# Kernel tuning notes

Hardware: AMD Instinct MI355X
Metric: run time of the kernel (lower is better)

## Reference

```python
import jax, jax.numpy as jnp
import numpy as np

B, N, D, C, NCLS = 8, 2048, 256, 128, 50
EPS = 1e-5  # BatchNorm eps

def _bn(x, g, b):
    # eval-mode BatchNorm1d over channel dim of (B,C,N): running_mean=0, running_var=1
    return x * (g / jnp.sqrt(1.0 + EPS))[:, None] + b[:, None]

def _complex_linear(x, Wr, br, Wi, bi):
    # torch ComplexLinear: complex(fr(x.real)-fi(x.imag), fr(x.imag)+fi(x.real))
    xr, xi = x.real, x.imag
    re = (xr @ Wr.T + br) - (xi @ Wi.T + bi)
    im = (xi @ Wr.T + br) + (xr @ Wi.T + bi)
    return jax.lax.complex(re, im)

def _sa(x, qkW, vW, vb, tW, tb, g, b):
    # x: (B,C,N); q/k share weights (tied in torch), dim C//4
    xq = jnp.einsum('qc,bcn->bnq', qkW, x)            # (B,N,C/4)
    xk = jnp.einsum('qc,bcm->bqm', qkW, x)            # (B,C/4,N)
    energy = jnp.einsum('bnq,bqm->bnm', xq, xk)       # (B,N,N)
    attn = jax.nn.softmax(energy, axis=-1)
    attn = attn / (1e-9 + attn.sum(axis=1, keepdims=True))  # column renorm
    xv = jnp.einsum('oc,bcn->bon', vW, x) + vb[:, None]
    xr = x - jnp.einsum('bcn,bnm->bcm', xv, attn)
    xr = jnp.einsum('oc,bcn->bon', tW, xr) + tb[:, None]
    return x + jax.nn.relu(_bn(xr, g, b))

def reference(xyz, cls_label, A, Bmat, W1r, b1r, W1i, b1i, W2r, b2r, W2i, b2i,
              lbl_emb, ft_w1, ft_g1, ft_b1, ft_w2, ft_g2, ft_b2,
              sa_qk, sa_vw, sa_vb, sa_tw, sa_tb, sa_g, sa_b,
              fuse_w, fuse_g, fuse_b, c1_w, c1_b, bn1_g, bn1_b, c2_w, c2_b):
    pts = xyz.transpose(0, 2, 1)                       # (B,N,3)
    # VecKM(d=256, alpha=30, beta=9): G = eB (eB^H eA), normalized to sqrt(d)
    eA = jnp.exp(1j * (pts @ A))                       # (B,N,D) complex64
    eB = jnp.exp(1j * (pts @ Bmat))
    inner = jnp.einsum('bnd,bne->bde', eB.conj(), eA)  # (B,D,D)
    G = jnp.einsum('bnd,bde->bne', eB, inner)          # (B,N,D)
    G = G / jnp.linalg.norm(G, axis=-1, keepdims=True) * jnp.sqrt(jnp.float32(D))
    G = _complex_linear(G, W1r, b1r, W1i, b1i)
    G = jax.lax.complex(jax.nn.relu(G.real), jax.nn.relu(G.imag))  # ComplexReLU
    G = _complex_linear(G, W2r, b2r, W2i, b2i)
    G = (G.real ** 2 + G.imag ** 2).transpose(0, 2, 1)  # (B,D,N)
    reweight = (cls_label @ lbl_emb)[:, :, None]        # (B,D,1)
    x = G * reweight
    x = jax.nn.relu(_bn(jnp.einsum('oc,bcn->bon', ft_w1, x), ft_g1, ft_b1))
    x = _bn(jnp.einsum('oc,bcn->bon', ft_w2, x), ft_g2, ft_b2)  # (B,C,N)
    feats = []
    for i in range(4):
        x = _sa(x, sa_qk[i], sa_vw[i], sa_vb[i], sa_tw[i], sa_tb[i], sa_g[i], sa_b[i])
        feats.append(x)
    x = jnp.concatenate(feats, axis=1)                  # (B,4C,N)
    x = jax.nn.relu(_bn(jnp.einsum('oc,bcn->bon', fuse_w, x), fuse_g, fuse_b))
    x = jax.nn.relu(_bn(jnp.einsum('oc,bcn->bon', c1_w, x) + c1_b[:, None], bn1_g, bn1_b))
    # dropout is identity in eval mode
    x = jnp.einsum('oc,bcn->bon', c2_w, x) + c2_b[:, None]
    x = jax.nn.log_softmax(x, axis=1)
    return x.transpose(0, 2, 1)                         # (B,N,NCLS)

def setup_inputs():
    key = jax.random.key(0)
    k = jax.random.split(key, 24)
    rn = lambda i, s: jax.random.normal(k[i], s, jnp.float32)
    s = 0.05
    return {
        'xyz': rn(0, (B, 3, N)),
        'cls_label': jax.random.uniform(k[1], (B, 16), jnp.float32),
        'A': rn(2, (3, D)) * 30.0,
        'Bmat': rn(3, (3, D)) * 9.0,
        'W1r': rn(4, (D, D)) * s, 'b1r': rn(5, (D,)) * s,
        'W1i': rn(6, (D, D)) * s, 'b1i': rn(7, (D,)) * s,
        'W2r': rn(8, (D, D)) * s, 'b2r': rn(9, (D,)) * s,
        'W2i': rn(10, (D, D)) * s, 'b2i': rn(11, (D,)) * s,
        'lbl_emb': rn(12, (16, D)),
        'ft_w1': rn(13, (C, D)) * s, 'ft_g1': jnp.ones((C,)), 'ft_b1': jnp.zeros((C,)),
        'ft_w2': rn(14, (C, C)) * s, 'ft_g2': jnp.ones((C,)), 'ft_b2': jnp.zeros((C,)),
        'sa_qk': rn(15, (4, C // 4, C)) * s,
        'sa_vw': rn(16, (4, C, C)) * s, 'sa_vb': rn(17, (4, C)) * s,
        'sa_tw': rn(18, (4, C, C)) * s, 'sa_tb': rn(19, (4, C)) * s,
        'sa_g': jnp.ones((4, C)), 'sa_b': jnp.zeros((4, C)),
        'fuse_w': rn(20, (C, 4 * C)) * s, 'fuse_g': jnp.ones((C,)), 'fuse_b': jnp.zeros((C,)),
        'c1_w': rn(21, (C, C)) * s, 'c1_b': rn(22, (C,)) * s,
        'bn1_g': jnp.ones((C,)), 'bn1_b': jnp.zeros((C,)),
        'c2_w': rn(23, (NCLS, C)) * s, 'c2_b': jnp.zeros((NCLS,)),
    }
```

## Files before the change

kernel.cpp:

```cpp
#include <hip/hip_runtime.h>

#define BB 8
#define NPTS 2048
#define DD 256
#define CCH 128
#define NCLASS 50
#define LOG2E 1.4426950408889634f

typedef __attribute__((ext_vector_type(8))) short short8;
typedef __attribute__((ext_vector_type(4))) float f32x4;
typedef unsigned short u16;
#define MFMA16(a,b,c) __builtin_amdgcn_mfma_f32_16x16x32_bf16(a,b,c,0,0,0)

__device__ __forceinline__ u16 f2bf(float x){
  union { float f; unsigned int u; } v; v.f = x;
  unsigned int r = v.u + 0x7FFFu + ((v.u >> 16) & 1u);
  return (u16)(r >> 16);
}
__device__ __forceinline__ float bf2f(u16 u){
  union { unsigned int u32; float f; } v; v.u32 = ((unsigned int)u) << 16; return v.f;
}
__device__ __forceinline__ void split2(float x, u16& h, u16& l){
  h = f2bf(x); l = f2bf(x - bf2f(h));
}
__device__ __forceinline__ short8 ld8(const u16* p){ return *(const short8*)p; }
__device__ __forceinline__ short8 zero8(){ short8 z = {0,0,0,0,0,0,0,0}; return z; }
__device__ __forceinline__ void split8(const float* v, short8& H, short8& L){
  #pragma unroll
  for (int i = 0; i < 8; i++) { u16 h, l; split2(v[i], h, l); H[i] = (short)h; L[i] = (short)l; }
}

struct WSplit {
  const float* src[12];
  int cnt[12];
  int off[12];
};
__global__ __launch_bounds__(256) void wsplit_kernel(WSplit wsp, u16* __restrict__ H,
                                                     u16* __restrict__ L)
{
  int seg = blockIdx.y;
  int idx = blockIdx.x*256 + threadIdx.x;
  if (idx >= wsp.cnt[seg]) return;
  float v = wsp.src[seg][idx];
  u16 h, l; split2(v, h, l);
  H[wsp.off[seg]+idx] = h; L[wsp.off[seg]+idx] = l;
}

__global__ __launch_bounds__(256) void ek1_kernel(
    const float* __restrict__ xyz, const float* __restrict__ A, const float* __restrict__ Bm,
    u16* __restrict__ ATrh, u16* __restrict__ ATrl, u16* __restrict__ ATih, u16* __restrict__ ATil,
    u16* __restrict__ BTrh, u16* __restrict__ BTrl, u16* __restrict__ BTih, u16* __restrict__ BTil)
{
  size_t idx = (size_t)blockIdx.x*256 + threadIdx.x;
  int n = (int)(idx & (NPTS-1));
  int d = (int)((idx >> 11) & (DD-1));
  int b = (int)(idx >> 19);
  float p0 = xyz[((size_t)b*3+0)*NPTS+n];
  float p1 = xyz[((size_t)b*3+1)*NPTS+n];
  float p2 = xyz[((size_t)b*3+2)*NPTS+n];
  float phA = p0*A[d] + p1*A[DD+d] + p2*A[2*DD+d];
  float phB = p0*Bm[d] + p1*Bm[DD+d] + p2*Bm[2*DD+d];
  float sa, ca, sb, cb;
  sincosf(phA, &sa, &ca);
  sincosf(phB, &sb, &cb);
  size_t off = ((size_t)b*DD + d)*NPTS + n;
  u16 h, l;
  split2(ca, h, l); ATrh[off] = h; ATrl[off] = l;
  split2(sa, h, l); ATih[off] = h; ATil[off] = l;
  split2(cb, h, l); BTrh[off] = h; BTrl[off] = l;
  split2(sb, h, l); BTih[off] = h; BTil[off] = l;
}

__global__ __launch_bounds__(256) void ek2_kernel(
    const float* __restrict__ xyz, const float* __restrict__ Bm,
    u16* __restrict__ Brh, u16* __restrict__ Brl, u16* __restrict__ Bih, u16* __restrict__ Bil)
{
  size_t idx = (size_t)blockIdx.x*256 + threadIdx.x;
  int d = (int)(idx & (DD-1));
  int n = (int)((idx >> 8) & (NPTS-1));
  int b = (int)(idx >> 19);
  float p0 = xyz[((size_t)b*3+0)*NPTS+n];
  float p1 = xyz[((size_t)b*3+1)*NPTS+n];
  float p2 = xyz[((size_t)b*3+2)*NPTS+n];
  float phB = p0*Bm[d] + p1*Bm[DD+d] + p2*Bm[2*DD+d];
  float sb, cb;
  sincosf(phB, &sb, &cb);
  size_t off = ((size_t)b*NPTS + n)*DD + d;
  u16 h, l;
  split2(cb, h, l); Brh[off] = h; Brl[off] = l;
  split2(sb, h, l); Bih[off] = h; Bil[off] = l;
}

__global__ __launch_bounds__(256) void inner_mfma_kernel(
    const u16* __restrict__ ATrh, const u16* __restrict__ ATrl,
    const u16* __restrict__ ATih, const u16* __restrict__ ATil,
    const u16* __restrict__ BTrh, const u16* __restrict__ BTrl,
    const u16* __restrict__ BTih, const u16* __restrict__ BTil,
    float2* __restrict__ PART)
{
  int z = blockIdx.z; int b = z & 7; int ch = z >> 3;
  int e0 = blockIdx.y*64, d0 = blockIdx.x*64;
  int tid = threadIdx.x, lane = tid & 63, w = tid >> 6;
  int wr = (w >> 1)*32, wc = (w & 1)*32;
  int r16 = lane & 15, g4 = lane >> 4;
  f32x4 re[2][2] = {}, ip[2][2] = {}, iq[2][2] = {};
  size_t ar_[2], br_[2];
  #pragma unroll
  for (int rg = 0; rg < 2; rg++) {
    ar_[rg] = ((size_t)b*DD + (e0 + wr + rg*16 + r16))*NPTS + g4*8;
    br_[rg] = ((size_t)b*DD + (d0 + wc + rg*16 + r16))*NPTS + g4*8;
  }
  int kbeg = ch*512, kend = kbeg + 512;
  for (int k0 = kbeg; k0 < kend; k0 += 32) {
    short8 arh[2], arl[2], aih[2], ail[2], brh[2], brl[2], bih[2], bil[2];
    #pragma unroll
    for (int rg = 0; rg < 2; rg++) {
      arh[rg] = ld8(ATrh + ar_[rg] + k0); arl[rg] = ld8(ATrl + ar_[rg] + k0);
      aih[rg] = ld8(ATih + ar_[rg] + k0); ail[rg] = ld8(ATil + ar_[rg] + k0);
      brh[rg] = ld8(BTrh + br_[rg] + k0); brl[rg] = ld8(BTrl + br_[rg] + k0);
      bih[rg] = ld8(BTih + br_[rg] + k0); bil[rg] = ld8(BTil + br_[rg] + k0);
    }
    #pragma unroll
    for (int ra = 0; ra < 2; ra++)
      #pragma unroll
      for (int rb = 0; rb < 2; rb++) {
        re[ra][rb] = MFMA16(arh[ra], brh[rb], re[ra][rb]);
        re[ra][rb] = MFMA16(arh[ra], brl[rb], re[ra][rb]);
        re[ra][rb] = MFMA16(arl[ra], brh[rb], re[ra][rb]);
        re[ra][rb] = MFMA16(aih[ra], bih[rb], re[ra][rb]);
        re[ra][rb] = MFMA16(aih[ra], bil[rb], re[ra][rb]);
        re[ra][rb] = MFMA16(ail[ra], bih[rb], re[ra][rb]);
        ip[ra][rb] = MFMA16(aih[ra], brh[rb], ip[ra][rb]);
        ip[ra][rb] = MFMA16(aih[ra], brl[rb], ip[ra][rb]);
        ip[ra][rb] = MFMA16(ail[ra], brh[rb], ip[ra][rb]);
        iq[ra][rb] = MFMA16(arh[ra], bih[rb], iq[ra][rb]);
        iq[ra][rb] = MFMA16(arh[ra], bil[rb], iq[ra][rb]);
        iq[ra][rb] = MFMA16(arl[ra], bih[rb], iq[ra][rb]);
      }
  }
  float2* outp = PART + ((size_t)(ch*BB + b)*DD)*DD;
  #pragma unroll
  for (int ra = 0; ra < 2; ra++)
    #pragma unroll
    for (int rb = 0; rb < 2; rb++)
      #pragma unroll
      for (int j = 0; j < 4; j++) {
        int e = e0 + wr + ra*16 + g4*4 + j;
        int d = d0 + wc + rb*16 + r16;
        outp[(size_t)e*DD + d] = make_float2(re[ra][rb][j], ip[ra][rb][j] - iq[ra][rb][j]);
      }
}

__global__ __launch_bounds__(256) void innred_kernel(const float2* __restrict__ P,
    u16* __restrict__ Irh, u16* __restrict__ Irl, u16* __restrict__ Iih, u16* __restrict__ Iil)
{
  size_t i = (size_t)blockIdx.x*256 + threadIdx.x;
  const size_t S = (size_t)BB*DD*DD;
  float2 a = P[i], b = P[i+S], c = P[i+2*S], d = P[i+3*S];
  float rr = a.x+b.x+c.x+d.x, ii = a.y+b.y+c.y+d.y;
  u16 h, l;
  split2(rr, h, l); Irh[i] = h; Irl[i] = l;
  split2(ii, h, l); Iih[i] = h; Iil[i] = l;
}

__global__ __launch_bounds__(256) void g_mfma_kernel(
    const u16* __restrict__ Brh, const u16* __restrict__ Brl,
    const u16* __restrict__ Bih, const u16* __restrict__ Bil,
    const u16* __restrict__ Irh, const u16* __restrict__ Irl,
    const u16* __restrict__ Iih, const u16* __restrict__ Iil,
    float2* __restrict__ G)
{
  int b = blockIdx.z;
  int n0 = blockIdx.y*64, e0 = blockIdx.x*64;
  int tid = threadIdx.x, lane = tid & 63, w = tid >> 6;
  int wr = (w >> 1)*32, wc = (w & 1)*32;
  int r16 = lane & 15, g4 = lane >> 4;
  f32x4 p[2][2] = {}, q[2][2] = {}, im[2][2] = {};
  size_t ar_[2], br_[2];
  #pragma unroll
  for (int rg = 0; rg < 2; rg++) {
    ar_[rg] = ((size_t)b*NPTS + (n0 + wr + rg*16 + r16))*DD + g4*8;
    br_[rg] = ((size_t)b*DD + (e0 + wc + rg*16 + r16))*DD + g4*8;
  }
  for (int k0 = 0; k0 < DD; k0 += 32) {
    short8 arh[2], arl[2], aih[2], ail[2], brh[2], brl[2], bih[2], bil[2];
    #pragma unroll
    for (int rg = 0; rg < 2; rg++) {
      arh[rg] = ld8(Brh + ar_[rg] + k0); arl[rg] = ld8(Brl + ar_[rg] + k0);
      aih[rg] = ld8(Bih + ar_[rg] + k0); ail[rg] = ld8(Bil + ar_[rg] + k0);
      brh[rg] = ld8(Irh + br_[rg] + k0); brl[rg] = ld8(Irl + br_[rg] + k0);
      bih[rg] = ld8(Iih + br_[rg] + k0); bil[rg] = ld8(Iil + br_[rg] + k0);
    }
    #pragma unroll
    for (int ra = 0; ra < 2; ra++)
      #pragma unroll
      for (int rb = 0; rb < 2; rb++) {
        p[ra][rb] = MFMA16(arh[ra], brh[rb], p[ra][rb]);
        p[ra][rb] = MFMA16(arh[ra], brl[rb], p[ra][rb]);
        p[ra][rb] = MFMA16(arl[ra], brh[rb], p[ra][rb]);
        q[ra][rb] = MFMA16(aih[ra], bih[rb], q[ra][rb]);
        q[ra][rb] = MFMA16(aih[ra], bil[rb], q[ra][rb]);
        q[ra][rb] = MFMA16(ail[ra], bih[rb], q[ra][rb]);
        im[ra][rb] = MFMA16(arh[ra], bih[rb], im[ra][rb]);
        im[ra][rb] = MFMA16(arh[ra], bil[rb], im[ra][rb]);
        im[ra][rb] = MFMA16(arl[ra], bih[rb], im[ra][rb]);
        im[ra][rb] = MFMA16(aih[ra], brh[rb], im[ra][rb]);
        im[ra][rb] = MFMA16(aih[ra], brl[rb], im[ra][rb]);
        im[ra][rb] = MFMA16(ail[ra], brh[rb], im[ra][rb]);
      }
  }
  #pragma unroll
  for (int ra = 0; ra < 2; ra++)
    #pragma unroll
    for (int rb = 0; rb < 2; rb++)
      #pragma unroll
      for (int j = 0; j < 4; j++) {
        int n = n0 + wr + ra*16 + g4*4 + j;
        int e = e0 + wc + rb*16 + r16;
        G[((size_t)b*NPTS + n)*DD + e] = make_float2(p[ra][rb][j] - q[ra][rb][j], im[ra][rb][j]);
      }
}

__global__ __launch_bounds__(256) void gnorm_kernel(float2* __restrict__ G)
{
  size_t row = blockIdx.x;
  float2* p = G + row*DD;
  int tid = threadIdx.x;
  float2 v = p[tid];
  __shared__ float red[256];
  red[tid] = v.x*v.x + v.y*v.y;
  __syncthreads();
  for (int w = 128; w > 0; w >>= 1) { if (tid < w) red[tid] += red[tid+w]; __syncthreads(); }
  float sc = 16.f * rsqrtf(red[0]);
  p[tid] = make_float2(v.x*sc, v.y*sc);
}

__global__ __launch_bounds__(256) void clinear_mfma_kernel(
    const float2* __restrict__ IN,
    const u16* __restrict__ Wrh, const u16* __restrict__ Wrl,
    const u16* __restrict__ Wih, const u16* __restrict__ Wil,
    const float* __restrict__ br, const float* __restrict__ bi,
    float2* __restrict__ OUT, int do_relu)
{
  int m0 = blockIdx.y*64, o0 = blockIdx.x*64;
  int tid = threadIdx.x, lane = tid & 63, w = tid >> 6;
  int wr = (w >> 1)*32, wc = (w & 1)*32;
  int r16 = lane & 15, g4 = lane >> 4;
  f32x4 p[2][2] = {}, q[2][2] = {}, im[2][2] = {};
  int mrow[2], orow[2];
  #pragma unroll
  for (int rg = 0; rg < 2; rg++) {
    mrow[rg] = m0 + wr + rg*16 + r16;
    orow[rg] = o0 + wc + rg*16 + r16;
  }
  for (int k0 = 0; k0 < DD; k0 += 32) {
    short8 arh[2], arl[2], aih[2], ail[2], brh[2], brl[2], bih[2], bil[2];
    #pragma unroll
    for (int rg = 0; rg < 2; rg++) {
      const float2* pa = IN + (size_t)mrow[rg]*DD + k0 + g4*8;
      float vr[8], vi[8];
      #pragma unroll
      for (int j = 0; j < 8; j++) { float2 t = pa[j]; vr[j] = t.x; vi[j] = t.y; }
      split8(vr, arh[rg], arl[rg]); split8(vi, aih[rg], ail[rg]);
      size_t wo = (size_t)orow[rg]*DD + k0 + g4*8;
      brh[rg] = ld8(Wrh + wo); brl[rg] = ld8(Wrl + wo);
      bih[rg] = ld8(Wih + wo); bil[rg] = ld8(Wil + wo);
    }
    #pragma unroll
    for (int ra = 0; ra < 2; ra++)
      #pragma unroll
      for (int rb = 0; rb < 2; rb++) {
        p[ra][rb] = MFMA16(arh[ra], brh[rb], p[ra][rb]);
        p[ra][rb] = MFMA16(arh[ra], brl[rb], p[ra][rb]);
        p[ra][rb] = MFMA16(arl[ra], brh[rb], p[ra][rb]);
        q[ra][rb] = MFMA16(aih[ra], bih[rb], q[ra][rb]);
        q[ra][rb] = MFMA16(aih[ra], bil[rb], q[ra][rb]);
        q[ra][rb] = MFMA16(ail[ra], bih[rb], q[ra][rb]);
        im[ra][rb] = MFMA16(arh[ra], bih[rb], im[ra][rb]);
        im[ra][rb] = MFMA16(arh[ra], bil[rb], im[ra][rb]);
        im[ra][rb] = MFMA16(arl[ra], bih[rb], im[ra][rb]);
        im[ra][rb] = MFMA16(aih[ra], brh[rb], im[ra][rb]);
        im[ra][rb] = MFMA16(aih[ra], brl[rb], im[ra][rb]);
        im[ra][rb] = MFMA16(ail[ra], brh[rb], im[ra][rb]);
      }
  }
  #pragma unroll
  for (int ra = 0; ra < 2; ra++)
    #pragma unroll
    for (int rb = 0; rb < 2; rb++)
      #pragma unroll
      for (int j = 0; j < 4; j++) {
        int m = m0 + wr + ra*16 + g4*4 + j;
        int o = o0 + wc + rb*16 + r16;
        float brv = br[o], biv = bi[o];
        float re = p[ra][rb][j] - q[ra][rb][j] + brv - biv;
        float iv = im[ra][rb][j] + brv + biv;
        if (do_relu) { re = fmaxf(re, 0.f); iv = fmaxf(iv, 0.f); }
        OUT[(size_t)m*DD + o] = make_float2(re, iv);
      }
}

__global__ void rw_kernel(const float* __restrict__ cls, const float* __restrict__ lbl,
                          float* __restrict__ RW)
{
  int b = blockIdx.x; int d = threadIdx.x;
  float s = 0.f;
  #pragma unroll
  for (int k = 0; k < 16; k++) s += cls[b*16+k] * lbl[k*DD+d];
  RW[b*DD+d] = s;
}

__global__ __launch_bounds__(256) void gsq_kernel(
    const float2* __restrict__ G, const float* __restrict__ RW, float* __restrict__ OUT)
{
  size_t idx = (size_t)blockIdx.x*256 + threadIdx.x;
  int d = (int)(idx & (DD-1));
  size_t bn = idx >> 8;
  int n = (int)(bn & (NPTS-1));
  int b = (int)(bn >> 11);
  float2 g = G[idx];
  OUT[((size_t)b*DD + d)*NPTS + n] = (g.x*g.x + g.y*g.y) * RW[b*DD+d];
}

__global__ __launch_bounds__(256) void sgemm_kernel(
    const u16* __restrict__ Wh, const u16* __restrict__ Wl,
    const float* __restrict__ X, float* __restrict__ Y,
    const float* __restrict__ RES,
    const float* __restrict__ bias, const float* __restrict__ bng, const float* __restrict__ bnb,
    u16* __restrict__ YBh, u16* __restrict__ YBl, int ybmode,
    int O, int Cin, size_t xbs, size_t ybs, size_t rbs, int flags)
{
  int b = blockIdx.z;
  int n0 = blockIdx.x*64, o0 = blockIdx.y*64;
  const float* x = X + (size_t)b*xbs;
  __shared__ u16 sXh[64][40], sXl[64][40];
  int tid = threadIdx.x, lane = tid & 63, w = tid >> 6;
  int wo = (w >> 1)*32, wn = (w & 1)*32;
  int r16 = lane & 15, g4 = lane >> 4;
  f32x4 acc[2][2] = {};
  int stc = tid >> 3;
  int stn = (tid & 7)*8;
  for (int k0 = 0; k0 < Cin; k0 += 32) {
    const float* px = x + (size_t)(k0+stc)*NPTS + n0 + stn;
    float4 u0 = *(const float4*)px;
    float4 u1 = *(const float4*)(px+4);
    float v[8] = {u0.x,u0.y,u0.z,u0.w,u1.x,u1.y,u1.z,u1.w};
    __syncthreads();
    #pragma unroll
    for (int j = 0; j < 8; j++) {
      u16 h, l; split2(v[j], h, l);
      sXh[stn+j][stc] = h; sXl[stn+j][stc] = l;
    }
    __syncthreads();
    short8 awh[2], awl[2], bxh[2], bxl[2];
    #pragma unroll
    for (int rg = 0; rg < 2; rg++) {
      int orow = o0 + wo + rg*16 + r16;
      if (orow < O) {
        size_t woff = (size_t)orow*Cin + k0 + g4*8;
        awh[rg] = ld8(Wh + woff); awl[rg] = ld8(Wl + woff);
      } else { awh[rg] = zero8(); awl[rg] = zero8(); }
      bxh[rg] = ld8(&sXh[wn + rg*16 + r16][g4*8]);
      bxl[rg] = ld8(&sXl[wn + rg*16 + r16][g4*8]);
    }
    #pragma unroll
    for (int ra = 0; ra < 2; ra++)
      #pragma unroll
      for (int rb = 0; rb < 2; rb++) {
        acc[ra][rb] = MFMA16(awh[ra], bxh[rb], acc[ra][rb]);
        acc[ra][rb] = MFMA16(awh[ra], bxl[rb], acc[ra][rb]);
        acc[ra][rb] = MFMA16(awl[ra], bxh[rb], acc[ra][rb]);
      }
  }
  #pragma unroll
  for (int ra = 0; ra < 2; ra++)
    #pragma unroll
    for (int rb = 0; rb < 2; rb++)
      #pragma unroll
      for (int j = 0; j < 4; j++) {
        int o = o0 + wo + ra*16 + g4*4 + j;
        if (o >= O) continue;
        int n = n0 + wn + rb*16 + r16;
        float v = acc[ra][rb][j];
        if (flags & 1) v += bias[o];
        if (flags & 2) v = v * (bng[o] * rsqrtf(1.f + 1e-5f)) + bnb[o];
        if (flags & 4) v = fmaxf(v, 0.f);
        if (flags & 8) v += RES[(size_t)b*rbs + (size_t)o*NPTS + n];
        if (ybmode == 0) Y[(size_t)b*ybs + (size_t)o*NPTS + n] = v;
        else if (ybmode == 1) YBh[(size_t)b*ybs + (size_t)o*NPTS + n] = f2bf(v);
        else {
          u16 h, l; split2(v, h, l);
          size_t off = ((size_t)b*NPTS + n)*32 + o;
          YBh[off] = h; YBl[off] = l;
        }
      }
}

__global__ __launch_bounds__(256) void sastat_kernel(
    const u16* __restrict__ Qh, const u16* __restrict__ Ql,
    float* __restrict__ PM, float* __restrict__ PS)
{
  int b = blockIdx.z, ch = blockIdx.y;
  int n0 = blockIdx.x*64;
  size_t base = (size_t)b*NPTS*32;
  int tid = threadIdx.x, lane = tid & 63, wid = tid >> 6;
  int r16 = lane & 15, g4 = lane >> 4;
  size_t ao = base + (size_t)(n0 + wid*16 + r16)*32 + g4*8;
  short8 ah = ld8(Qh + ao), al = ld8(Ql + ao);
  float pm[4] = {-3.4e38f,-3.4e38f,-3.4e38f,-3.4e38f};
  float ps[4] = {0.f,0.f,0.f,0.f};
  int mbeg = ch*512, mend = mbeg + 512;
  for (int mt = mbeg; mt < mend; mt += 32) {
    size_t bo0 = base + (size_t)(mt + r16)*32 + g4*8;
    size_t bo1 = bo0 + 16*32;
    short8 bh0 = ld8(Qh+bo0), bl0 = ld8(Ql+bo0);
    short8 bh1 = ld8(Qh+bo1), bl1 = ld8(Ql+bo1);
    f32x4 a0 = {}, a1 = {};
    a0 = MFMA16(ah, bh0, a0); a0 = MFMA16(ah, bl0, a0); a0 = MFMA16(al, bh0, a0);
    a1 = MFMA16(ah, bh1, a1); a1 = MFMA16(ah, bl1, a1); a1 = MFMA16(al, bh1, a1);
    #pragma unroll
    for (int j = 0; j < 4; j++) {
      float v = fmaxf(a0[j], a1[j]);
      float mn = fmaxf(pm[j], v);
      ps[j] = ps[j]*exp2f((pm[j]-mn)*LOG2E)
            + exp2f((a0[j]-mn)*LOG2E) + exp2f((a1[j]-mn)*LOG2E);
      pm[j] = mn;
    }
  }
  #pragma unroll
  for (int j = 0; j < 4; j++) {
    float m = pm[j], s = ps[j];
    #pragma unroll
    for (int d = 1; d < 16; d <<= 1) {
      float om = __shfl_xor(m, d);
      float os = __shfl_xor(s, d);
      float mn = fmaxf(m, om);
      s = s*exp2f((m-mn)*LOG2E) + os*exp2f((om-mn)*LOG2E);
      m = mn;
    }
    if (r16 == 0) {
      int n_ = n0 + wid*16 + g4*4 + j;
      size_t off = ((size_t)ch*BB + b)*NPTS + n_;
      PM[off] = m; PS[off] = s;
    }
  }
}

__global__ __launch_bounds__(256) void comb1_kernel(
    const float* __restrict__ PM, const float* __restrict__ PS,
    float* __restrict__ MX, float* __restrict__ RS)
{
  size_t i = (size_t)blockIdx.x*256 + threadIdx.x;
  const size_t S = (size_t)BB*NPTS;
  float m0 = PM[i], m1 = PM[i+S], m2 = PM[i+2*S], m3 = PM[i+3*S];
  float mx = fmaxf(fmaxf(m0,m1), fmaxf(m2,m3));
  float den = PS[i]*exp2f((m0-mx)*LOG2E) + PS[i+S]*exp2f((m1-mx)*LOG2E)
            + PS[i+2*S]*exp2f((m2-mx)*LOG2E) + PS[i+3*S]*exp2f((m3-mx)*LOG2E);
  MX[i] = mx; RS[i] = 1.f/den;
}

__global__ __launch_bounds__(256) void saattn_kernel(
    const u16* __restrict__ Qh, const u16* __restrict__ Ql,
    const float* __restrict__ MX, const float* __restrict__ RS,
    u16* __restrict__ AT, float* __restrict__ CSP)
{
  int b = blockIdx.z, ch = blockIdx.y;
  int m0 = blockIdx.x*64;
  size_t base = (size_t)b*NPTS*32;
  const float* mx = MX + (size_t)b*NPTS;
  const float* rs = RS + (size_t)b*NPTS;
  u16* at = AT + (size_t)b*NPTS*NPTS;
  __shared__ u16 lds[4][16][40];
  int tid = threadIdx.x, lane = tid & 63, wid = tid >> 6;
  int r16 = lane & 15, g4 = lane >> 4;
  size_t ao = base + (size_t)(m0 + wid*16 + r16)*32 + g4*8;
  short8 ah = ld8(Qh + ao), al = ld8(Ql + ao);
  float csum[4] = {0.f,0.f,0.f,0.f};
  int srow = lane >> 2, soct = (lane & 3)*8;
  int nbeg = ch*512, nend = nbeg + 512;
  for (int nt = nbeg; nt < nend; nt += 32) {
    size_t bo0 = base + (size_t)(nt + r16)*32 + g4*8;
    size_t bo1 = bo0 + 16*32;
    short8 bh0 = ld8(Qh+bo0), bl0 = ld8(Ql+bo0);
    short8 bh1 = ld8(Qh+bo1), bl1 = ld8(Ql+bo1);
    f32x4 a0 = {}, a1 = {};
    a0 = MFMA16(ah, bh0, a0); a0 = MFMA16(ah, bl0, a0); a0 = MFMA16(al, bh0, a0);
    a1 = MFMA16(ah, bh1, a1); a1 = MFMA16(ah, bl1, a1); a1 = MFMA16(al, bh1, a1);
    int nc0 = nt + r16, nc1 = nc0 + 16;
    float mx0 = mx[nc0], rs0 = rs[nc0], mx1 = mx[nc1], rs1 = rs[nc1];
    #pragma unroll
    for (int j = 0; j < 4; j++) {
      float t0 = exp2f((a0[j]-mx0)*LOG2E)*rs0;
      float t1 = exp2f((a1[j]-mx1)*LOG2E)*rs1;
      csum[j] += t0 + t1;
      lds[wid][g4*4+j][r16] = f2bf(t0);
      lds[wid][g4*4+j][r16+16] = f2bf(t1);
    }
    __syncthreads();
    short8 row = *(const short8*)&lds[wid][srow][soct];
    *(short8*)(at + (size_t)(m0 + wid*16 + srow)*NPTS + nt + soct) = row;
    __syncthreads();
  }
  #pragma unroll
  for (int j = 0; j < 4; j++) {
    float c = csum[j];
    #pragma unroll
    for (int d = 1; d < 16; d <<= 1) c += __shfl_xor(c, d);
    if (r16 == 0) {
      int m_ = m0 + wid*16 + g4*4 + j;
      CSP[((size_t)ch*BB + b)*NPTS + m_] = c;
    }
  }
}

__global__ __launch_bounds__(256) void comb2_kernel(const float* __restrict__ CSP,
                                                    float* __restrict__ CSI)
{
  size_t i = (size_t)blockIdx.x*256 + threadIdx.x;
  const size_t S = (size_t)BB*NPTS;
  CSI[i] = 1.f/(1e-9f + CSP[i] + CSP[i+S] + CSP[i+2*S] + CSP[i+3*S]);
}

__global__ __launch_bounds__(256) void apply_mfma_kernel(
    const u16* __restrict__ XV, const u16* __restrict__ AT,
    const float* __restrict__ CSI, const float* __restrict__ XRES, size_t res_bs,
    float* __restrict__ OUT)
{
  int b = blockIdx.z;
  int m0 = blockIdx.x*64;
  int c0 = blockIdx.y*64;
  const u16* xv = XV + (size_t)b*CCH*NPTS;
  const u16* at = AT + (size_t)b*NPTS*NPTS;
  int tid = threadIdx.x, lane = tid & 63, w = tid >> 6;
  int wc = c0 + (w >> 1)*32, wm = (w & 1)*32;
  int r16 = lane & 15, g4 = lane >> 4;
  f32x4 acc[2][2] = {};
  const u16* pa0 = xv + (size_t)(wc + r16)*NPTS + g4*8;
  const u16* pa1 = pa0 + (size_t)16*NPTS;
  const u16* pb0 = at + (size_t)(m0 + wm + r16)*NPTS + g4*8;
  const u16* pb1 = pb0 + (size_t)16*NPTS;
  for (int k0 = 0; k0 < NPTS; k0 += 32) {
    short8 a0 = ld8(pa0 + k0);
    short8 a1 = ld8(pa1 + k0);
    short8 b0 = ld8(pb0 + k0);
    short8 b1 = ld8(pb1 + k0);
    acc[0][0] = MFMA16(a0, b0, acc[0][0]);
    acc[0][1] = MFMA16(a0, b1, acc[0][1]);
    acc[1][0] = MFMA16(a1, b0, acc[1][0]);
    acc[1][1] = MFMA16(a1, b1, acc[1][1]);
  }
  #pragma unroll
  for (int ca = 0; ca < 2; ca++)
    #pragma unroll
    for (int mb = 0; mb < 2; mb++) {
      int m = m0 + wm + mb*16 + r16;
      float ci = CSI[(size_t)b*NPTS + m];
      #pragma unroll
      for (int j = 0; j < 4; j++) {
        int c = wc + ca*16 + g4*4 + j;
        float v = XRES[(size_t)b*res_bs + (size_t)c*NPTS + m] - acc[ca][mb][j]*ci;
        OUT[((size_t)b*CCH + c)*NPTS + m] = v;
      }
    }
}

__global__ __launch_bounds__(256) void lsm_kernel(const float* __restrict__ Y,
                                                  float* __restrict__ OUT)
{
  int idx = blockIdx.x*256 + threadIdx.x;
  int b = idx >> 11, n = idx & (NPTS-1);
  const float* p = Y + (size_t)b*NCLASS*NPTS + n;
  float m = -3.4e38f;
  #pragma unroll
  for (int k = 0; k < NCLASS; k++) m = fmaxf(m, p[(size_t)k*NPTS]);
  float s = 0.f;
  #pragma unroll
  for (int k = 0; k < NCLASS; k++) s += expf(p[(size_t)k*NPTS] - m);
  float L = m + logf(s);
  float* o = OUT + (size_t)idx*NCLASS;
  #pragma unroll
  for (int k = 0; k < NCLASS; k++) o[k] = p[(size_t)k*NPTS] - L;
}

extern "C" void kernel_launch(void* const* d_in, const int* in_sizes, int n_in,
                              void* d_out, int out_size, void* d_ws, size_t ws_size,
                              hipStream_t stream)
{
  (void)in_sizes; (void)n_in; (void)out_size; (void)ws_size;
  const float* xyz  = (const float*)d_in[0];
  const float* cls  = (const float*)d_in[1];
  const float* Amat = (const float*)d_in[2];
  const float* Bm   = (const float*)d_in[3];
  const float* W1r  = (const float*)d_in[4];
  const float* b1r  = (const float*)d_in[5];
  const float* W1i  = (const float*)d_in[6];
  const float* b1i  = (const float*)d_in[7];
  const float* W2r  = (const float*)d_in[8];
  const float* b2r  = (const float*)d_in[9];
  const float* W2i  = (const float*)d_in[10];
  const float* b2i  = (const float*)d_in[11];
  const float* lbl  = (const float*)d_in[12];
  const float* ftw1 = (const float*)d_in[13];
  const float* ftg1 = (const float*)d_in[14];
  const float* ftb1 = (const float*)d_in[15];
  const float* ftw2 = (const float*)d_in[16];
  const float* ftg2 = (const float*)d_in[17];
  const float* ftb2 = (const float*)d_in[18];
  const float* saqk = (const float*)d_in[19];
  const float* savw = (const float*)d_in[20];
  const float* savb = (const float*)d_in[21];
  const float* satw = (const float*)d_in[22];
  const float* satb = (const float*)d_in[23];
  const float* sag  = (const float*)d_in[24];
  const float* sab  = (const float*)d_in[25];
  const float* fusew= (const float*)d_in[26];
  const float* fuseg= (const float*)d_in[27];
  const float* fuseb= (const float*)d_in[28];
  const float* c1w  = (const float*)d_in[29];
  const float* c1b  = (const float*)d_in[30];
  const float* bn1g = (const float*)d_in[31];
  const float* bn1b = (const float*)d_in[32];
  const float* c2w  = (const float*)d_in[33];
  const float* c2b  = (const float*)d_in[34];
  float* out = (float*)d_out;

  float* ws = (float*)d_ws;
  const size_t PS  = (size_t)BB*DD*NPTS;
  const size_t ISZ = (size_t)BB*DD*DD;
  u16* U = (u16*)ws;
  u16 *ATrh = U+0*PS, *ATrl = U+1*PS, *ATih = U+2*PS, *ATil = U+3*PS;
  u16 *BTrh = U+4*PS, *BTrl = U+5*PS, *BTih = U+6*PS, *BTil = U+7*PS;
  u16 *Bnrh = U+8*PS, *Bnrl = U+9*PS, *Bnih = U+10*PS, *Bnil = U+11*PS;
  u16 *Irh = U+12*PS, *Irl = U+12*PS+ISZ, *Iih = U+12*PS+2*ISZ, *Iil = U+12*PS+3*ISZ;
  float* gsq = (float*)(U + 12*PS + 4*ISZ);
  float2* PART = (float2*)gsq;
  float2* Gbuf1 = (float2*)ws;
  float2* Gbuf2 = (float2*)(U + 4*PS);
  u16* attnT = (u16*)ws;
  size_t p = (size_t)BB*NPTS*NPTS;
  float* xfeat = ws + p;  p += (size_t)BB*CCH*NPTS;
  float* feats = ws + p;  p += (size_t)BB*4*CCH*NPTS;
  float* xt1   = ws + p;  p += (size_t)BB*CCH*NPTS;
  float* xt2   = ws + p;  p += (size_t)BB*CCH*NPTS;
  float* ybuf  = ws + p;  p += (size_t)BB*NCLASS*NPTS;
  float* mxv   = ws + p;  p += (size_t)BB*NPTS;
  float* rsv   = ws + p;  p += (size_t)BB*NPTS;
  float* csi   = ws + p;  p += (size_t)BB*NPTS;
  float* rwb   = ws + p;  p += (size_t)BB*DD;
  float* PMb   = ws + p;  p += (size_t)4*BB*NPTS;
  float* PSb   = ws + p;  p += (size_t)4*BB*NPTS;
  float* CSPb  = ws + p;  p += (size_t)4*BB*NPTS;
  u16* xqh = (u16*)(ws + p);
  u16* xql = xqh + (size_t)BB*NPTS*32;
  u16* xvb = xql + (size_t)BB*NPTS*32;
  u16* wpH = xvb + (size_t)BB*CCH*NPTS;
  u16* wpL = wpH + 557056;

  const int o_w1r=0, o_w1i=65536, o_w2r=131072, o_w2i=196608, o_ft1=262144,
            o_ft2=294912, o_qk=311296, o_vw=327680, o_tw=393216, o_fu=458752,
            o_c1=524288, o_c2=540672;
  WSplit wsp;
  const float* srcs[12] = {W1r,W1i,W2r,W2i,ftw1,ftw2,saqk,savw,satw,fusew,c1w,c2w};
  const int cnts[12] = {65536,65536,65536,65536,32768,16384,16384,65536,65536,65536,16384,6400};
  const int offs[12] = {o_w1r,o_w1i,o_w2r,o_w2i,o_ft1,o_ft2,o_qk,o_vw,o_tw,o_fu,o_c1,o_c2};
  for (int i = 0; i < 12; i++) { wsp.src[i]=srcs[i]; wsp.cnt[i]=cnts[i]; wsp.off[i]=offs[i]; }

  wsplit_kernel<<<dim3(256, 12), 256, 0, stream>>>(wsp, wpH, wpL);
  ek1_kernel<<<(int)(PS/256), 256, 0, stream>>>(xyz, Amat, Bm,
      ATrh, ATrl, ATih, ATil, BTrh, BTrl, BTih, BTil);
  ek2_kernel<<<(int)(PS/256), 256, 0, stream>>>(xyz, Bm, Bnrh, Bnrl, Bnih, Bnil);
  inner_mfma_kernel<<<dim3(DD/64, DD/64, BB*4), 256, 0, stream>>>(
      ATrh, ATrl, ATih, ATil, BTrh, BTrl, BTih, BTil, PART);
  innred_kernel<<<(int)(ISZ/256), 256, 0, stream>>>(PART, Irh, Irl, Iih, Iil);
  g_mfma_kernel<<<dim3(DD/64, NPTS/64, BB), 256, 0, stream>>>(
      Bnrh, Bnrl, Bnih, Bnil, Irh, Irl, Iih, Iil, Gbuf1);
  gnorm_kernel<<<BB*NPTS, 256, 0, stream>>>(Gbuf1);
  clinear_mfma_kernel<<<dim3(DD/64, (BB*NPTS)/64), 256, 0, stream>>>(
      Gbuf1, wpH+o_w1r, wpL+o_w1r, wpH+o_w1i, wpL+o_w1i, b1r, b1i, Gbuf2, 1);
  clinear_mfma_kernel<<<dim3(DD/64, (BB*NPTS)/64), 256, 0, stream>>>(
      Gbuf2, wpH+o_w2r, wpL+o_w2r, wpH+o_w2i, wpL+o_w2i, b2r, b2i, Gbuf1, 0);
  rw_kernel<<<BB, DD, 0, stream>>>(cls, lbl, rwb);
  gsq_kernel<<<(int)(PS/256), 256, 0, stream>>>(Gbuf1, rwb, gsq);

  sgemm_kernel<<<dim3(NPTS/64, CCH/64, BB), 256, 0, stream>>>(
      wpH+o_ft1, wpL+o_ft1, gsq, xt1, nullptr, nullptr, ftg1, ftb1, nullptr, nullptr, 0,
      CCH, DD, (size_t)DD*NPTS, (size_t)CCH*NPTS, 0, 2|4);
  sgemm_kernel<<<dim3(NPTS/64, CCH/64, BB), 256, 0, stream>>>(
      wpH+o_ft2, wpL+o_ft2, xt1, xfeat, nullptr, nullptr, ftg2, ftb2, nullptr, nullptr, 0,
      CCH, CCH, (size_t)CCH*NPTS, (size_t)CCH*NPTS, 0, 2);

  const float* xsrc = xfeat;
  size_t xbs = (size_t)CCH*NPTS;
  for (int i = 0; i < 4; i++) {
    sgemm_kernel<<<dim3(NPTS/64, 1, BB), 256, 0, stream>>>(
        wpH+o_qk + i*32*CCH, wpL+o_qk + i*32*CCH, xsrc, nullptr, nullptr,
        nullptr, nullptr, nullptr, xqh, xql, 2, 32, CCH, xbs, 0, 0, 0);
    sastat_kernel<<<dim3(NPTS/64, 4, BB), 256, 0, stream>>>(xqh, xql, PMb, PSb);
    comb1_kernel<<<(BB*NPTS)/256, 256, 0, stream>>>(PMb, PSb, mxv, rsv);
    saattn_kernel<<<dim3(NPTS/64, 4, BB), 256, 0, stream>>>(xqh, xql, mxv, rsv, attnT, CSPb);
    comb2_kernel<<<(BB*NPTS)/256, 256, 0, stream>>>(CSPb, csi);
    sgemm_kernel<<<dim3(NPTS/64, CCH/64, BB), 256, 0, stream>>>(
        wpH+o_vw + i*CCH*CCH, wpL+o_vw + i*CCH*CCH, xsrc, nullptr, nullptr,
        savb + i*CCH, nullptr, nullptr, xvb, nullptr, 1, CCH, CCH, xbs,
        (size_t)CCH*NPTS, 0, 1);
    apply_mfma_kernel<<<dim3(NPTS/64, CCH/64, BB), 256, 0, stream>>>(
        xvb, attnT, csi, xsrc, xbs, xt2);
    sgemm_kernel<<<dim3(NPTS/64, CCH/64, BB), 256, 0, stream>>>(
        wpH+o_tw + i*CCH*CCH, wpL+o_tw + i*CCH*CCH, xt2, feats + (size_t)i*CCH*NPTS, xsrc,
        satb + i*CCH, sag + i*CCH, sab + i*CCH, nullptr, nullptr, 0,
        CCH, CCH, (size_t)CCH*NPTS, (size_t)4*CCH*NPTS, xbs, 1|2|4|8);
    xsrc = feats + (size_t)i*CCH*NPTS;
    xbs = (size_t)4*CCH*NPTS;
  }

  sgemm_kernel<<<dim3(NPTS/64, CCH/64, BB), 256, 0, stream>>>(
      wpH+o_fu, wpL+o_fu, feats, xt1, nullptr, nullptr, fuseg, fuseb, nullptr, nullptr, 0,
      CCH, 4*CCH, (size_t)4*CCH*NPTS, (size_t)CCH*NPTS, 0, 2|4);
  sgemm_kernel<<<dim3(NPTS/64, CCH/64, BB), 256, 0, stream>>>(
      wpH+o_c1, wpL+o_c1, xt1, xt2, nullptr, c1b, bn1g, bn1b, nullptr, nullptr, 0,
      CCH, CCH, (size_t)CCH*NPTS, (size_t)CCH*NPTS, 0, 1|2|4);
  sgemm_kernel<<<dim3(NPTS/64, 1, BB), 256, 0, stream>>>(
      wpH+o_c2, wpL+o_c2, xt2, ybuf, nullptr, c2b, nullptr, nullptr, nullptr, nullptr, 0,
      NCLASS, CCH, (size_t)CCH*NPTS, (size_t)NCLASS*NPTS, 0, 1);
  lsm_kernel<<<(BB*NPTS)/256, 256, 0, stream>>>(ybuf, out);
}
```

Measured before the change: 1.052 ms.

## Fuse bf16 splitting, gsq epilogue and softmax combine passes into neighbouring kernels

The G normalisation kernel now writes pre-split bf16 hi/lo planes, so the complex-linear kernels load bf16 operands directly instead of re-splitting fp32 inputs on every tile. The second complex linear computes the squared magnitude times the reweight in its epilogue, which removes the separate gsq pass and the float2 round trip. The comb1 and comb2 reductions are folded into saattn and apply through shared-memory prologues, removing eight small launches. In exchange, each saattn and apply block redundantly recomputes its slice of the combine statistics, and the split planes use more memory than the fp32 buffers.

```diff
diff --git a/kernel.cpp b/kernel.cpp
--- a/kernel.cpp
+++ b/kernel.cpp
@@ -25,10 +25,6 @@
 }
 __device__ __forceinline__ short8 ld8(const u16* p){ return *(const short8*)p; }
 __device__ __forceinline__ short8 zero8(){ short8 z = {0,0,0,0,0,0,0,0}; return z; }
-__device__ __forceinline__ void split8(const float* v, short8& H, short8& L){
-  #pragma unroll
-  for (int i = 0; i < 8; i++) { u16 h, l; split2(v[i], h, l); H[i] = (short)h; L[i] = (short)l; }
-}
 
 struct WSplit {
   const float* src[12];
@@ -221,10 +217,11 @@
       }
 }
 
-__global__ __launch_bounds__(256) void gnorm_kernel(float2* __restrict__ G)
+__global__ __launch_bounds__(256) void gnormsplit_kernel(const float2* __restrict__ Gf,
+    u16* __restrict__ Grh, u16* __restrict__ Grl, u16* __restrict__ Gih, u16* __restrict__ Gil)
 {
   size_t row = blockIdx.x;
-  float2* p = G + row*DD;
+  const float2* p = Gf + row*DD;
   int tid = threadIdx.x;
   float2 v = p[tid];
   __shared__ float red[256];
@@ -232,39 +229,40 @@
   __syncthreads();
   for (int w = 128; w > 0; w >>= 1) { if (tid < w) red[tid] += red[tid+w]; __syncthreads(); }
   float sc = 16.f * rsqrtf(red[0]);
-  p[tid] = make_float2(v.x*sc, v.y*sc);
+  size_t off = row*DD + tid;
+  u16 h, l;
+  split2(v.x*sc, h, l); Grh[off] = h; Grl[off] = l;
+  split2(v.y*sc, h, l); Gih[off] = h; Gil[off] = l;
 }
 
 __global__ __launch_bounds__(256) void clinear_mfma_kernel(
-    const float2* __restrict__ IN,
+    const u16* __restrict__ Arh, const u16* __restrict__ Arl,
+    const u16* __restrict__ Aih, const u16* __restrict__ Ail,
     const u16* __restrict__ Wrh, const u16* __restrict__ Wrl,
     const u16* __restrict__ Wih, const u16* __restrict__ Wil,
     const float* __restrict__ br, const float* __restrict__ bi,
-    float2* __restrict__ OUT, int do_relu)
+    u16* __restrict__ Orh, u16* __restrict__ Orl, u16* __restrict__ Oih, u16* __restrict__ Oil,
+    const float* __restrict__ RW, float* __restrict__ GSQ, int mode)
 {
   int m0 = blockIdx.y*64, o0 = blockIdx.x*64;
   int tid = threadIdx.x, lane = tid & 63, w = tid >> 6;
   int wr = (w >> 1)*32, wc = (w & 1)*32;
   int r16 = lane & 15, g4 = lane >> 4;
   f32x4 p[2][2] = {}, q[2][2] = {}, im[2][2] = {};
-  int mrow[2], orow[2];
+  size_t ar_[2], br_[2];
   #pragma unroll
   for (int rg = 0; rg < 2; rg++) {
-    mrow[rg] = m0 + wr + rg*16 + r16;
-    orow[rg] = o0 + wc + rg*16 + r16;
+    ar_[rg] = (size_t)(m0 + wr + rg*16 + r16)*DD + g4*8;
+    br_[rg] = (size_t)(o0 + wc + rg*16 + r16)*DD + g4*8;
   }
   for (int k0 = 0; k0 < DD; k0 += 32) {
     short8 arh[2], arl[2], aih[2], ail[2], brh[2], brl[2], bih[2], bil[2];
     #pragma unroll
     for (int rg = 0; rg < 2; rg++) {
-      const float2* pa = IN + (size_t)mrow[rg]*DD + k0 + g4*8;
-      float vr[8], vi[8];
-      #pragma unroll
-      for (int j = 0; j < 8; j++) { float2 t = pa[j]; vr[j] = t.x; vi[j] = t.y; }
-      split8(vr, arh[rg], arl[rg]); split8(vi, aih[rg], ail[rg]);
-      size_t wo = (size_t)orow[rg]*DD + k0 + g4*8;
-      brh[rg] = ld8(Wrh + wo); brl[rg] = ld8(Wrl + wo);
-      bih[rg] = ld8(Wih + wo); bil[rg] = ld8(Wil + wo);
+      arh[rg] = ld8(Arh + ar_[rg] + k0); arl[rg] = ld8(Arl + ar_[rg] + k0);
+      aih[rg] = ld8(Aih + ar_[rg] + k0); ail[rg] = ld8(Ail + ar_[rg] + k0);
+      brh[rg] = ld8(Wrh + br_[rg] + k0); brl[rg] = ld8(Wrl + br_[rg] + k0);
+      bih[rg] = ld8(Wih + br_[rg] + k0); bil[rg] = ld8(Wil + br_[rg] + k0);
     }
     #pragma unroll
     for (int ra = 0; ra < 2; ra++)
@@ -287,17 +285,34 @@
   #pragma unroll
   for (int ra = 0; ra < 2; ra++)
     #pragma unroll
-    for (int rb = 0; rb < 2; rb++)
-      #pragma unroll
-      for (int j = 0; j < 4; j++) {
-        int m = m0 + wr + ra*16 + g4*4 + j;
-        int o = o0 + wc + rb*16 + r16;
-        float brv = br[o], biv = bi[o];
-        float re = p[ra][rb][j] - q[ra][rb][j] + brv - biv;
-        float iv = im[ra][rb][j] + brv + biv;
-        if (do_relu) { re = fmaxf(re, 0.f); iv = fmaxf(iv, 0.f); }
-        OUT[(size_t)m*DD + o] = make_float2(re, iv);
-      }
+    for (int rb = 0; rb < 2; rb++) {
+      int o = o0 + wc + rb*16 + r16;
+      float brv = br[o], biv = bi[o];
+      if (mode == 1) {
+        #pragma unroll
+        for (int j = 0; j < 4; j++) {
+          int m = m0 + wr + ra*16 + g4*4 + j;
+          float re = fmaxf(p[ra][rb][j] - q[ra][rb][j] + brv - biv, 0.f);
+          float iv = fmaxf(im[ra][rb][j] + brv + biv, 0.f);
+          size_t off = (size_t)m*DD + o;
+          u16 h, l;
+          split2(re, h, l); Orh[off] = h; Orl[off] = l;
+          split2(iv, h, l); Oih[off] = h; Oil[off] = l;
+        }
+      } else {
+        int mbase = m0 + wr + ra*16 + g4*4;
+        int b = mbase >> 11, nb = mbase & (NPTS-1);
+        float rwv = RW[(size_t)b*DD + o];
+        float4 gv;
+        #pragma unroll
+        for (int j = 0; j < 4; j++) {
+          float re = p[ra][rb][j] - q[ra][rb][j] + brv - biv;
+          float iv = im[ra][rb][j] + brv + biv;
+          ((float*)&gv)[j] = (re*re + iv*iv) * rwv;
+        }
+        *(float4*)(GSQ + ((size_t)b*DD + o)*NPTS + nb) = gv;
+      }
+    }
 }
 
 __global__ void rw_kernel(const float* __restrict__ cls, const float* __restrict__ lbl,
@@ -308,18 +323,6 @@
   #pragma unroll
   for (int k = 0; k < 16; k++) s += cls[b*16+k] * lbl[k*DD+d];
   RW[b*DD+d] = s;
-}
-
-__global__ __launch_bounds__(256) void gsq_kernel(
-    const float2* __restrict__ G, const float* __restrict__ RW, float* __restrict__ OUT)
-{
-  size_t idx = (size_t)blockIdx.x*256 + threadIdx.x;
-  int d = (int)(idx & (DD-1));
-  size_t bn = idx >> 8;
-  int n = (int)(bn & (NPTS-1));
-  int b = (int)(bn >> 11);
-  float2 g = G[idx];
-  OUT[((size_t)b*DD + d)*NPTS + n] = (g.x*g.x + g.y*g.y) * RW[b*DD+d];
 }
 
 __global__ __launch_bounds__(256) void sgemm_kernel(
@@ -446,38 +449,34 @@
   }
 }
 
-__global__ __launch_bounds__(256) void comb1_kernel(
-    const float* __restrict__ PM, const float* __restrict__ PS,
-    float* __restrict__ MX, float* __restrict__ RS)
-{
-  size_t i = (size_t)blockIdx.x*256 + threadIdx.x;
-  const size_t S = (size_t)BB*NPTS;
-  float m0 = PM[i], m1 = PM[i+S], m2 = PM[i+2*S], m3 = PM[i+3*S];
-  float mx = fmaxf(fmaxf(m0,m1), fmaxf(m2,m3));
-  float den = PS[i]*exp2f((m0-mx)*LOG2E) + PS[i+S]*exp2f((m1-mx)*LOG2E)
-            + PS[i+2*S]*exp2f((m2-mx)*LOG2E) + PS[i+3*S]*exp2f((m3-mx)*LOG2E);
-  MX[i] = mx; RS[i] = 1.f/den;
-}
-
 __global__ __launch_bounds__(256) void saattn_kernel(
     const u16* __restrict__ Qh, const u16* __restrict__ Ql,
-    const float* __restrict__ MX, const float* __restrict__ RS,
+    const float* __restrict__ PM, const float* __restrict__ PS,
     u16* __restrict__ AT, float* __restrict__ CSP)
 {
   int b = blockIdx.z, ch = blockIdx.y;
   int m0 = blockIdx.x*64;
   size_t base = (size_t)b*NPTS*32;
-  const float* mx = MX + (size_t)b*NPTS;
-  const float* rs = RS + (size_t)b*NPTS;
   u16* at = AT + (size_t)b*NPTS*NPTS;
   __shared__ u16 lds[4][16][40];
+  __shared__ float smx[512], srs[512];
   int tid = threadIdx.x, lane = tid & 63, wid = tid >> 6;
   int r16 = lane & 15, g4 = lane >> 4;
+  int nbeg = ch*512, nend = nbeg + 512;
+  const size_t S = (size_t)BB*NPTS;
+  for (int t = tid; t < 512; t += 256) {
+    size_t bn = (size_t)b*NPTS + nbeg + t;
+    float m0_ = PM[bn], m1 = PM[S+bn], m2 = PM[2*S+bn], m3 = PM[3*S+bn];
+    float mxv = fmaxf(fmaxf(m0_,m1), fmaxf(m2,m3));
+    float den = PS[bn]*exp2f((m0_-mxv)*LOG2E) + PS[S+bn]*exp2f((m1-mxv)*LOG2E)
+              + PS[2*S+bn]*exp2f((m2-mxv)*LOG2E) + PS[3*S+bn]*exp2f((m3-mxv)*LOG2E);
+    smx[t] = mxv; srs[t] = 1.f/den;
+  }
+  __syncthreads();
   size_t ao = base + (size_t)(m0 + wid*16 + r16)*32 + g4*8;
   short8 ah = ld8(Qh + ao), al = ld8(Ql + ao);
   float csum[4] = {0.f,0.f,0.f,0.f};
   int srow = lane >> 2, soct = (lane & 3)*8;
-  int nbeg = ch*512, nend = nbeg + 512;
   for (int nt = nbeg; nt < nend; nt += 32) {
     size_t bo0 = base + (size_t)(nt + r16)*32 + g4*8;
     size_t bo1 = bo0 + 16*32;
@@ -486,8 +485,8 @@
     f32x4 a0 = {}, a1 = {};
     a0 = MFMA16(ah, bh0, a0); a0 = MFMA16(ah, bl0, a0); a0 = MFMA16(al, bh0, a0);
     a1 = MFMA16(ah, bh1, a1); a1 = MFMA16(ah, bl1, a1); a1 = MFMA16(al, bh1, a1);
-    int nc0 = nt + r16, nc1 = nc0 + 16;
-    float mx0 = mx[nc0], rs0 = rs[nc0], mx1 = mx[nc1], rs1 = rs[nc1];
+    int nl0 = nt - nbeg + r16, nl1 = nl0 + 16;
+    float mx0 = smx[nl0], rs0 = srs[nl0], mx1 = smx[nl1], rs1 = srs[nl1];
     #pragma unroll
     for (int j = 0; j < 4; j++) {
       float t0 = exp2f((a0[j]-mx0)*LOG2E)*rs0;
@@ -513,17 +512,9 @@
   }
 }
 
-__global__ __launch_bounds__(256) void comb2_kernel(const float* __restrict__ CSP,
-                                                    float* __restrict__ CSI)
-{
-  size_t i = (size_t)blockIdx.x*256 + threadIdx.x;
-  const size_t S = (size_t)BB*NPTS;
-  CSI[i] = 1.f/(1e-9f + CSP[i] + CSP[i+S] + CSP[i+2*S] + CSP[i+3*S]);
-}
-
 __global__ __launch_bounds__(256) void apply_mfma_kernel(
     const u16* __restrict__ XV, const u16* __restrict__ AT,
-    const float* __restrict__ CSI, const float* __restrict__ XRES, size_t res_bs,
+    const float* __restrict__ CSP, const float* __restrict__ XRES, size_t res_bs,
     float* __restrict__ OUT)
 {
   int b = blockIdx.z;
@@ -531,7 +522,15 @@
   int c0 = blockIdx.y*64;
   const u16* xv = XV + (size_t)b*CCH*NPTS;
   const u16* at = AT + (size_t)b*NPTS*NPTS;
+  __shared__ float scsi[64];
   int tid = threadIdx.x, lane = tid & 63, w = tid >> 6;
+  const size_t S = (size_t)BB*NPTS;
+  if (tid < 64) {
+    size_t bm = (size_t)b*NPTS + m0 + tid;
+    float c = CSP[bm] + CSP[S+bm] + CSP[2*S+bm] + CSP[3*S+bm];
+    scsi[tid] = 1.f/(1e-9f + c);
+  }
+  __syncthreads();
   int wc = c0 + (w >> 1)*32, wm = (w & 1)*32;
   int r16 = lane & 15, g4 = lane >> 4;
   f32x4 acc[2][2] = {};
@@ -554,7 +553,7 @@
     #pragma unroll
     for (int mb = 0; mb < 2; mb++) {
       int m = m0 + wm + mb*16 + r16;
-      float ci = CSI[(size_t)b*NPTS + m];
+      float ci = scsi[wm + mb*16 + r16];
       #pragma unroll
       for (int j = 0; j < 4; j++) {
         int c = wc + ca*16 + g4*4 + j;
@@ -634,8 +633,9 @@
   u16 *Irh = U+12*PS, *Irl = U+12*PS+ISZ, *Iih = U+12*PS+2*ISZ, *Iil = U+12*PS+3*ISZ;
   float* gsq = (float*)(U + 12*PS + 4*ISZ);
   float2* PART = (float2*)gsq;
-  float2* Gbuf1 = (float2*)ws;
-  float2* Gbuf2 = (float2*)(U + 4*PS);
+  float2* Gf = (float2*)ws;
+  u16 *G1rh = U+4*PS, *G1rl = U+5*PS, *G1ih = U+6*PS, *G1il = U+7*PS;
+  u16 *G2rh = U+8*PS, *G2rl = U+9*PS, *G2ih = U+10*PS, *G2il = U+11*PS;
   u16* attnT = (u16*)ws;
   size_t p = (size_t)BB*NPTS*NPTS;
   float* xfeat = ws + p;  p += (size_t)BB*CCH*NPTS;
@@ -643,9 +643,6 @@
   float* xt1   = ws + p;  p += (size_t)BB*CCH*NPTS;
   float* xt2   = ws + p;  p += (size_t)BB*CCH*NPTS;
   float* ybuf  = ws + p;  p += (size_t)BB*NCLASS*NPTS;
-  float* mxv   = ws + p;  p += (size_t)BB*NPTS;
-  float* rsv   = ws + p;  p += (size_t)BB*NPTS;
-  float* csi   = ws + p;  p += (size_t)BB*NPTS;
   float* rwb   = ws + p;  p += (size_t)BB*DD;
   float* PMb   = ws + p;  p += (size_t)4*BB*NPTS;
   float* PSb   = ws + p;  p += (size_t)4*BB*NPTS;
@@ -666,6 +663,7 @@
   for (int i = 0; i < 12; i++) { wsp.src[i]=srcs[i]; wsp.cnt[i]=cnts[i]; wsp.off[i]=offs[i]; }
 
   wsplit_kernel<<<dim3(256, 12), 256, 0, stream>>>(wsp, wpH, wpL);
+  rw_kernel<<<BB, DD, 0, stream>>>(cls, lbl, rwb);
   ek1_kernel<<<(int)(PS/256), 256, 0, stream>>>(xyz, Amat, Bm,
       ATrh, ATrl, ATih, ATil, BTrh, BTrl, BTih, BTil);
   ek2_kernel<<<(int)(PS/256), 256, 0, stream>>>(xyz, Bm, Bnrh, Bnrl, Bnih, Bnil);
@@ -673,14 +671,14 @@
       ATrh, ATrl, ATih, ATil, BTrh, BTrl, BTih, BTil, PART);
   innred_kernel<<<(int)(ISZ/256), 256, 0, stream>>>(PART, Irh, Irl, Iih, Iil);
   g_mfma_kernel<<<dim3(DD/64, NPTS/64, BB), 256, 0, stream>>>(
-      Bnrh, Bnrl, Bnih, Bnil, Irh, Irl, Iih, Iil, Gbuf1);
-  gnorm_kernel<<<BB*NPTS, 256, 0, stream>>>(Gbuf1);
+      Bnrh, Bnrl, Bnih, Bnil, Irh, Irl, Iih, Iil, Gf);
+  gnormsplit_kernel<<<BB*NPTS, 256, 0, stream>>>(Gf, G1rh, G1rl, G1ih, G1il);
   clinear_mfma_kernel<<<dim3(DD/64, (BB*NPTS)/64), 256, 0, stream>>>(
-      Gbuf1, wpH+o_w1r, wpL+o_w1r, wpH+o_w1i, wpL+o_w1i, b1r, b1i, Gbuf2, 1);
+      G1rh, G1rl, G1ih, G1il, wpH+o_w1r, wpL+o_w1r, wpH+o_w1i, wpL+o_w1i,
+      b1r, b1i, G2rh, G2rl, G2ih, G2il, nullptr, nullptr, 1);
   clinear_mfma_kernel<<<dim3(DD/64, (BB*NPTS)/64), 256, 0, stream>>>(
-      Gbuf2, wpH+o_w2r, wpL+o_w2r, wpH+o_w2i, wpL+o_w2i, b2r, b2i, Gbuf1, 0);
-  rw_kernel<<<BB, DD, 0, stream>>>(cls, lbl, rwb);
-  gsq_kernel<<<(int)(PS/256), 256, 0, stream>>>(Gbuf1, rwb, gsq);
+      G2rh, G2rl, G2ih, G2il, wpH+o_w2r, wpL+o_w2r, wpH+o_w2i, wpL+o_w2i,
+      b2r, b2i, nullptr, nullptr, nullptr, nullptr, rwb, gsq, 2);
 
   sgemm_kernel<<<dim3(NPTS/64, CCH/64, BB), 256, 0, stream>>>(
       wpH+o_ft1, wpL+o_ft1, gsq, xt1, nullptr, nullptr, ftg1, ftb1, nullptr, nullptr, 0,
@@ -696,15 +694,13 @@
         wpH+o_qk + i*32*CCH, wpL+o_qk + i*32*CCH, xsrc, nullptr, nullptr,
         nullptr, nullptr, nullptr, xqh, xql, 2, 32, CCH, xbs, 0, 0, 0);
     sastat_kernel<<<dim3(NPTS/64, 4, BB), 256, 0, stream>>>(xqh, xql, PMb, PSb);
-    comb1_kernel<<<(BB*NPTS)/256, 256, 0, stream>>>(PMb, PSb, mxv, rsv);
-    saattn_kernel<<<dim3(NPTS/64, 4, BB), 256, 0, stream>>>(xqh, xql, mxv, rsv, attnT, CSPb);
-    comb2_kernel<<<(BB*NPTS)/256, 256, 0, stream>>>(CSPb, csi);
+    saattn_kernel<<<dim3(NPTS/64, 4, BB), 256, 0, stream>>>(xqh, xql, PMb, PSb, attnT, CSPb);
     sgemm_kernel<<<dim3(NPTS/64, CCH/64, BB), 256, 0, stream>>>(
         wpH+o_vw + i*CCH*CCH, wpL+o_vw + i*CCH*CCH, xsrc, nullptr, nullptr,
         savb + i*CCH, nullptr, nullptr, xvb, nullptr, 1, CCH, CCH, xbs,
         (size_t)CCH*NPTS, 0, 1);
     apply_mfma_kernel<<<dim3(NPTS/64, CCH/64, BB), 256, 0, stream>>>(
-        xvb, attnT, csi, xsrc, xbs, xt2);
+        xvb, attnT, CSPb, xsrc, xbs, xt2);
     sgemm_kernel<<<dim3(NPTS/64, CCH/64, BB), 256, 0, stream>>>(
         wpH+o_tw + i*CCH*CCH, wpL+o_tw + i*CCH*CCH, xt2, feats + (size_t)i*CCH*NPTS, xsrc,
         satb + i*CCH, sag + i*CCH, sab + i*CCH, nullptr, nullptr, 0,
```

Result: faster. 998.7 us (-5.1%).
